# Kernel optimization log

Hardware: AMD Instinct MI355X
Metric: run time of the kernel (lower is better)

Reference implementation:

```python
import jax, jax.numpy as jnp
import numpy as np

D = 2048          # in_features == out_features (d_model)
H_TOTAL = 8192    # hidden_features, split across experts
E = 8             # num_experts
K = 2             # num_selects (top-k)
HE = H_TOTAL // E # per-expert hidden size
B, S = 2, 2048


def setup_inputs() -> dict:
    key = jax.random.key(0)
    ks = jax.random.split(key, 8)
    scale_up = 1.0 / np.sqrt(D)
    scale_dn = 1.0 / np.sqrt(HE)
    return {
        "x": jax.random.normal(ks[0], (B, S, D), dtype=jnp.float32),
        # mlp gate network: Linear(D,E,no bias) -> tanh -> Linear(E,E,no bias)
        "Wg1": jax.random.normal(ks[1], (E, D), dtype=jnp.float32) * 0.02,
        "Wg2": jax.random.normal(ks[2], (E, E), dtype=jnp.float32) * 0.2,
        # per-expert GLU-MLP weights (stacked over expert axis)
        "Wup": jax.random.uniform(ks[3], (E, HE, D), dtype=jnp.float32, minval=-scale_up, maxval=scale_up),
        "bup": jax.random.uniform(ks[4], (E, HE), dtype=jnp.float32, minval=-scale_up, maxval=scale_up),
        "Wdown": jax.random.uniform(ks[5], (E, D, HE), dtype=jnp.float32, minval=-scale_dn, maxval=scale_dn),
        "bdown": jax.random.uniform(ks[6], (E, D), dtype=jnp.float32, minval=-scale_dn, maxval=scale_dn),
    }


def reference(x, Wg1, Wg2, Wup, bup, Wdown, bdown):
    Bd, Sd, Dd = x.shape
    T = Bd * Sd
    xt = x.reshape(T, Dd)                                   # [T, D] tokens

    # ---- TopKBalancedNoisyGate (eval mode: no noise) ----
    logits = jnp.tanh(xt @ Wg1.T) @ Wg2.T                   # [T, E]
    _, top_idx = jax.lax.top_k(logits, K)                   # [T, K]
    top_logits = jnp.take_along_axis(logits, top_idx, axis=1)
    top_scores = jax.nn.softmax(top_logits.astype(jnp.float32), axis=1).astype(logits.dtype)
    # scatter top-k scores into dense [T, E] (zeros elsewhere)
    rows = jnp.arange(T)[:, None]
    scores = jnp.zeros_like(logits).at[rows, top_idx].set(top_scores)

    # ---- per-expert Linear-GLU experts: up -> silu -> down, score-combined ----
    up = jnp.einsum('td,ehd->teh', xt, Wup) + bup           # [T, E, HE]
    h = jax.nn.silu(up)
    down = jnp.einsum('teh,eoh->teo', h, Wdown) + bdown     # [T, E, D]
    out = jnp.einsum('te,teo->to', scores, down)            # [T, D]
    return out.reshape(Bd, Sd, Dd)
```

## Files before the change

### kernel.cpp

```cpp
#include <hip/hip_runtime.h>
#include <hip/hip_bf16.h>

#define D_DIM 2048
#define HE_DIM 1024
#define E_NUM 8
#define T_NUM 4096
#define TK_NUM 8192
#define TILE 128
#define BK 64
#define MAXROWS 9216
#define MAXMT 72

#define M_CNT(e)  ((e) * 32)
#define M_FILL(e) (256 + (e) * 32)
#define M_OFF  512
#define M_NMT  520
#define M_TE   528
#define M_TB   600
#define M_INTS 1024

typedef unsigned short u16;
typedef __attribute__((ext_vector_type(8))) short bf16x8;
typedef __attribute__((ext_vector_type(4))) float f32x4;

#define OFF_XB   ((size_t)0)
#define OFF_WUPB (OFF_XB + (size_t)T_NUM * D_DIM * 2)
#define OFF_SLOT ((size_t)0)
#define OFF_WDNB (OFF_WUPB + (size_t)E_NUM * HE_DIM * D_DIM * 2)
#define OFF_H    (OFF_WDNB + (size_t)E_NUM * D_DIM * HE_DIM * 2)
#define OFF_SCR  (OFF_H + (size_t)MAXROWS * HE_DIM * 2)
#define OFF_EIDX (OFF_SCR + (size_t)TK_NUM * 4)
#define OFF_RT   (OFF_EIDX + (size_t)TK_NUM * 4)
#define OFF_RS   (OFF_RT + (size_t)MAXROWS * 4)
#define OFF_META (OFF_RS + (size_t)MAXROWS * 4)

__device__ __forceinline__ u16 f2bf(float f) {
  unsigned u = __float_as_uint(f);
  u += 0x7FFFu + ((u >> 16) & 1u);
  return (u16)(u >> 16);
}
__device__ __forceinline__ float bf_lo(unsigned u) { return __uint_as_float(u << 16); }
__device__ __forceinline__ float bf_hi(unsigned u) { return __uint_as_float(u & 0xFFFF0000u); }

__device__ __forceinline__ void gload16(const void* g, void* l) {
  __builtin_amdgcn_global_load_lds((const __attribute__((address_space(1))) void*)g,
                                   (__attribute__((address_space(3))) void*)l,
                                   16, 0, 0);
}

__global__ void k_init(int* __restrict__ meta, int* __restrict__ rows_slot,
                       float* __restrict__ rowscore) {
  int i = blockIdx.x * blockDim.x + threadIdx.x;
  if (i < M_INTS) meta[i] = 0;
  if (i < MAXROWS) { rows_slot[i] = -1; rowscore[i] = 0.0f; }
}

__global__ void k_cvt2(const float4* __restrict__ s1, const float4* __restrict__ s2,
                       ushort4* __restrict__ d1, ushort4* __restrict__ d2, int n4) {
  int i = blockIdx.x * blockDim.x + threadIdx.x;
  int st = gridDim.x * blockDim.x;
  for (; i < 2 * n4; i += st) {
    const float4* s = (i < n4) ? s1 : s2;
    ushort4* d = (i < n4) ? d1 : d2;
    int j = (i < n4) ? i : i - n4;
    float4 v = s[j];
    ushort4 o;
    o.x = f2bf(v.x); o.y = f2bf(v.y); o.z = f2bf(v.z); o.w = f2bf(v.w);
    d[j] = o;
  }
}

__global__ __launch_bounds__(256) void k_gate(
    const float4* __restrict__ x4, const float4* __restrict__ Wg1_4,
    const float* __restrict__ Wg2, ushort4* __restrict__ xb4,
    int* __restrict__ eidx, float* __restrict__ scr, int* __restrict__ meta) {
  __shared__ float4 wg1s[E_NUM * (D_DIM / 4)];
  __shared__ int cnt_s[E_NUM];
  const int tid = threadIdx.x;
  if (tid < E_NUM) cnt_s[tid] = 0;
#pragma unroll
  for (int i = 0; i < 16; ++i) wg1s[tid + i * 256] = Wg1_4[tid + i * 256];
  __syncthreads();

  const int w = tid >> 6;
  const int lane = tid & 63;
  for (int j = 0; j < 4; ++j) {
    const int t = blockIdx.x * 16 + w * 4 + j;
    float acc[E_NUM];
#pragma unroll
    for (int e = 0; e < E_NUM; ++e) acc[e] = 0.f;
#pragma unroll
    for (int i = 0; i < 8; ++i) {
      const int c = lane + i * 64;
      float4 xv = x4[(size_t)t * 512 + c];
      ushort4 o;
      o.x = f2bf(xv.x); o.y = f2bf(xv.y); o.z = f2bf(xv.z); o.w = f2bf(xv.w);
      xb4[(size_t)t * 512 + c] = o;
#pragma unroll
      for (int e = 0; e < E_NUM; ++e) {
        float4 wv = wg1s[e * 512 + c];
        acc[e] += xv.x * wv.x + xv.y * wv.y + xv.z * wv.z + xv.w * wv.w;
      }
    }
#pragma unroll
    for (int e = 0; e < E_NUM; ++e) {
      float v = acc[e];
#pragma unroll
      for (int off = 32; off; off >>= 1) v += __shfl_xor(v, off, 64);
      acc[e] = v;
    }
    if (lane == 0) {
      float l1[E_NUM], lg[E_NUM];
#pragma unroll
      for (int e = 0; e < E_NUM; ++e) l1[e] = tanhf(acc[e]);
#pragma unroll
      for (int i = 0; i < E_NUM; ++i) {
        float s = 0.f;
#pragma unroll
        for (int e = 0; e < E_NUM; ++e) s += l1[e] * Wg2[i * E_NUM + e];
        lg[i] = s;
      }
      int i0 = 0; float v0 = lg[0];
#pragma unroll
      for (int i = 1; i < E_NUM; ++i) if (lg[i] > v0) { v0 = lg[i]; i0 = i; }
      int i1 = -1; float v1 = -3.4e38f;
#pragma unroll
      for (int i = 0; i < E_NUM; ++i) if (i != i0 && lg[i] > v1) { v1 = lg[i]; i1 = i; }
      float e1 = __expf(v1 - v0);
      float s0 = 1.f / (1.f + e1);
      float s1 = e1 * s0;
      eidx[t * 2] = i0; eidx[t * 2 + 1] = i1;
      scr[t * 2] = s0;  scr[t * 2 + 1] = s1;
      atomicAdd(&cnt_s[i0], 1);
      atomicAdd(&cnt_s[i1], 1);
    }
  }
  __syncthreads();
  if (tid < E_NUM) atomicAdd(&meta[M_CNT(tid)], cnt_s[tid]);
}

__global__ void k_offsets(int* __restrict__ meta) {
  const int lane = threadIdx.x;
  int cnt = (lane < E_NUM) ? meta[M_CNT(lane)] : 0;
  int tiles = (cnt + TILE - 1) / TILE;
  int pre = tiles;
#pragma unroll
  for (int off = 1; off < E_NUM; off <<= 1) {
    int v = __shfl_up(pre, off, 64);
    if (lane >= off && lane < E_NUM) pre += v;
  }
  int tb_excl = pre - tiles;
  if (lane < E_NUM) meta[M_OFF + lane] = tb_excl * TILE;
  const int nmt = __shfl(pre, E_NUM - 1, 64);
  if (lane == 0) meta[M_NMT] = nmt;
  int tb[E_NUM];
#pragma unroll
  for (int k = 0; k < E_NUM; ++k) tb[k] = __shfl(tb_excl, k, 64);
  for (int mt = lane; mt < nmt; mt += 64) {
    int e = 0;
#pragma unroll
    for (int k = 1; k < E_NUM; ++k) if (mt >= tb[k]) e = k;
    meta[M_TE + mt] = e;
    meta[M_TB + mt] = mt * TILE;
  }
}

__global__ void k_assign(const int* __restrict__ eidx, const float* __restrict__ scr,
                         int* __restrict__ meta, int* __restrict__ rows_slot,
                         float* __restrict__ rowscore) {
  int i = blockIdx.x * blockDim.x + threadIdx.x;
  const int lane = threadIdx.x & 63;
  int e = eidx[i];
  int pos = 0;
#pragma unroll
  for (int ex = 0; ex < E_NUM; ++ex) {
    unsigned long long m = __ballot(e == ex);
    if (e == ex) {
      int leader = __ffsll((long long)m) - 1;
      int rank = __popcll(m & ((1ull << lane) - 1ull));
      int b = 0;
      if (lane == leader) b = atomicAdd(&meta[M_FILL(ex)], __popcll(m));
      b = __shfl(b, leader, 64);
      pos = b + rank;
    }
  }
  int r = meta[M_OFF + e] + pos;
  rows_slot[r] = i;
  rowscore[r] = scr[i];
}

__global__ __launch_bounds__(256) void k_up(
    const u16* __restrict__ xb, const u16* __restrict__ wupb,
    const float* __restrict__ bup, const int* __restrict__ meta,
    const int* __restrict__ rows_slot, u16* __restrict__ hbuf) {
  const int mt = blockIdx.y;
  if (mt >= meta[M_NMT]) return;
  const int e = meta[M_TE + mt];
  const int mbase = meta[M_TB + mt];
  const int nt = blockIdx.x;

  __shared__ u16 As[TILE * BK];
  __shared__ u16 Bs[TILE * BK];

  const int tid = threadIdx.x;
  const int lane = tid & 63;
  const int w = tid >> 6;
  const int r0 = tid >> 3;
  const int cb = (((tid & 7) ^ ((tid >> 3) & 7)) * 8);

  const u16* gA[4];
  const u16* gB[4];
#pragma unroll
  for (int j = 0; j < 4; ++j) {
    int s = rows_slot[mbase + r0 + 32 * j]; if (s < 0) s = 0;
    gA[j] = xb + (size_t)(s >> 1) * D_DIM + cb;
    gB[j] = wupb + ((size_t)e * HE_DIM + nt * TILE + r0 + 32 * j) * D_DIM + cb;
  }
  u16* lA = As + tid * 8;
  u16* lB = Bs + tid * 8;

  const int wm = (w & 1) * 64;
  const int wn = (w >> 1) * 64;
  const int quad = lane >> 4;
  const int l16 = lane & 15;
  const int sw = l16 & 7;
  const u16* pa0 = As + (wm + l16) * BK;
  const u16* pb0 = Bs + (wn + l16) * BK;

  f32x4 acc[4][4] = {};

  for (int k0 = 0; k0 < D_DIM; k0 += BK) {
#pragma unroll
    for (int j = 0; j < 4; ++j) gload16(gA[j] + k0, lA + 2048 * j);
#pragma unroll
    for (int j = 0; j < 4; ++j) gload16(gB[j] + k0, lB + 2048 * j);
    __syncthreads();
#pragma unroll
    for (int h = 0; h < 2; ++h) {
      const int off = ((h * 4 + quad) ^ sw) * 8;
      bf16x8 af[4], bfr[4];
#pragma unroll
      for (int i = 0; i < 4; ++i) {
        af[i]  = *(const bf16x8*)(pa0 + i * 16 * BK + off);
        bfr[i] = *(const bf16x8*)(pb0 + i * 16 * BK + off);
      }
#pragma unroll
      for (int mi = 0; mi < 4; ++mi)
#pragma unroll
        for (int ni = 0; ni < 4; ++ni)
          acc[mi][ni] = __builtin_amdgcn_mfma_f32_16x16x32_bf16(af[mi], bfr[ni], acc[mi][ni], 0, 0, 0);
    }
    __syncthreads();
  }

#pragma unroll
  for (int mi = 0; mi < 4; ++mi) {
    const int m = wm + mi * 16 + quad * 4;
#pragma unroll
    for (int ni = 0; ni < 4; ++ni) {
      const int ng = nt * TILE + wn + ni * 16 + l16;
      const float bias = bup[e * HE_DIM + ng];
#pragma unroll
      for (int r = 0; r < 4; ++r) {
        float v = acc[mi][ni][r] + bias;
        v = v / (1.0f + __expf(-v));
        hbuf[(size_t)(mbase + m + r) * HE_DIM + ng] = f2bf(v);
      }
    }
  }
}

__global__ __launch_bounds__(256) void k_down(
    const u16* __restrict__ hbuf, const u16* __restrict__ wdnb,
    const float* __restrict__ bdown, const int* __restrict__ meta,
    const int* __restrict__ rows_slot, const float* __restrict__ rowscore,
    u16* __restrict__ slot) {
  const int mt = blockIdx.y;
  if (mt >= meta[M_NMT]) return;
  const int e = meta[M_TE + mt];
  const int mbase = meta[M_TB + mt];
  const int nt = blockIdx.x;

  __shared__ u16 As[TILE * BK];
  __shared__ u16 Bs[TILE * BK];

  const int tid = threadIdx.x;
  const int lane = tid & 63;
  const int w = tid >> 6;
  const int r0 = tid >> 3;
  const int cb = (((tid & 7) ^ ((tid >> 3) & 7)) * 8);

  const u16* gA[4];
  const u16* gB[4];
#pragma unroll
  for (int j = 0; j < 4; ++j) {
    gA[j] = hbuf + (size_t)(mbase + r0 + 32 * j) * HE_DIM + cb;
    gB[j] = wdnb + ((size_t)e * D_DIM + nt * TILE + r0 + 32 * j) * HE_DIM + cb;
  }
  u16* lA = As + tid * 8;
  u16* lB = Bs + tid * 8;

  const int wm = (w & 1) * 64;
  const int wn = (w >> 1) * 64;
  const int quad = lane >> 4;
  const int l16 = lane & 15;
  const int sw = l16 & 7;
  const u16* pa0 = As + (wm + l16) * BK;
  const u16* pb0 = Bs + (wn + l16) * BK;

  f32x4 acc[4][4] = {};

  for (int k0 = 0; k0 < HE_DIM; k0 += BK) {
#pragma unroll
    for (int j = 0; j < 4; ++j) gload16(gA[j] + k0, lA + 2048 * j);
#pragma unroll
    for (int j = 0; j < 4; ++j) gload16(gB[j] + k0, lB + 2048 * j);
    __syncthreads();
#pragma unroll
    for (int h = 0; h < 2; ++h) {
      const int off = ((h * 4 + quad) ^ sw) * 8;
      bf16x8 af[4], bfr[4];
#pragma unroll
      for (int i = 0; i < 4; ++i) {
        af[i]  = *(const bf16x8*)(pa0 + i * 16 * BK + off);
        bfr[i] = *(const bf16x8*)(pb0 + i * 16 * BK + off);
      }
#pragma unroll
      for (int mi = 0; mi < 4; ++mi)
#pragma unroll
        for (int ni = 0; ni < 4; ++ni)
          acc[mi][ni] = __builtin_amdgcn_mfma_f32_16x16x32_bf16(af[mi], bfr[ni], acc[mi][ni], 0, 0, 0);
    }
    __syncthreads();
  }

#pragma unroll
  for (int mi = 0; mi < 4; ++mi) {
    const int m = wm + mi * 16 + quad * 4;
#pragma unroll
    for (int r = 0; r < 4; ++r) {
      const int rg = mbase + m + r;
      const int s = rows_slot[rg];
      const float sc = rowscore[rg];
      if (s < 0) continue;
      u16* dst = slot + (size_t)s * D_DIM;
#pragma unroll
      for (int ni = 0; ni < 4; ++ni) {
        const int ng = nt * TILE + wn + ni * 16 + l16;
        float v = (acc[mi][ni][r] + bdown[e * D_DIM + ng]) * sc;
        dst[ng] = f2bf(v);
      }
    }
  }
}

__global__ __launch_bounds__(256) void k_combine(const u16* __restrict__ slot,
                                                 float* __restrict__ out) {
  int i = blockIdx.x * blockDim.x + threadIdx.x;
  int t = i >> 8;
  int c = i & 255;
  const uint4* p0 = (const uint4*)(slot + (size_t)(t * 2) * D_DIM) + c;
  const uint4* p1 = (const uint4*)(slot + (size_t)(t * 2 + 1) * D_DIM) + c;
  uint4 a = *p0, b = *p1;
  float4 o0, o1;
  o0.x = bf_lo(a.x) + bf_lo(b.x);  o0.y = bf_hi(a.x) + bf_hi(b.x);
  o0.z = bf_lo(a.y) + bf_lo(b.y);  o0.w = bf_hi(a.y) + bf_hi(b.y);
  o1.x = bf_lo(a.z) + bf_lo(b.z);  o1.y = bf_hi(a.z) + bf_hi(b.z);
  o1.z = bf_lo(a.w) + bf_lo(b.w);  o1.w = bf_hi(a.w) + bf_hi(b.w);
  float4* po = (float4*)(out + (size_t)t * D_DIM) + c * 2;
  po[0] = o0;
  po[1] = o1;
}

extern "C" void kernel_launch(void* const* d_in, const int* in_sizes, int n_in,
                              void* d_out, int out_size, void* d_ws, size_t ws_size,
                              hipStream_t stream) {
  const float* x     = (const float*)d_in[0];
  const float* Wg1   = (const float*)d_in[1];
  const float* Wg2   = (const float*)d_in[2];
  const float* Wup   = (const float*)d_in[3];
  const float* bup   = (const float*)d_in[4];
  const float* Wdown = (const float*)d_in[5];
  const float* bdown = (const float*)d_in[6];
  float* out = (float*)d_out;

  char* ws = (char*)d_ws;
  u16*   xb         = (u16*)(ws + OFF_XB);
  u16*   wupb       = (u16*)(ws + OFF_WUPB);
  u16*   wdnb       = (u16*)(ws + OFF_WDNB);
  u16*   hbuf       = (u16*)(ws + OFF_H);
  u16*   slotbuf    = (u16*)(ws + OFF_SLOT);
  float* scr        = (float*)(ws + OFF_SCR);
  int*   eidx       = (int*)(ws + OFF_EIDX);
  int*   rows_slot  = (int*)(ws + OFF_RT);
  float* rowscore   = (float*)(ws + OFF_RS);
  int*   meta       = (int*)(ws + OFF_META);

  k_init<<<(MAXROWS + 255) / 256, 256, 0, stream>>>(meta, rows_slot, rowscore);
  k_cvt2<<<8192, 256, 0, stream>>>((const float4*)Wup, (const float4*)Wdown,
                                   (ushort4*)wupb, (ushort4*)wdnb,
                                   E_NUM * HE_DIM * D_DIM / 4);
  k_gate<<<T_NUM / 16, 256, 0, stream>>>((const float4*)x, (const float4*)Wg1, Wg2,
                                         (ushort4*)xb, eidx, scr, meta);
  k_offsets<<<1, 64, 0, stream>>>(meta);
  k_assign<<<TK_NUM / 256, 256, 0, stream>>>(eidx, scr, meta, rows_slot, rowscore);
  k_up<<<dim3(HE_DIM / TILE, MAXMT), 256, 0, stream>>>(xb, wupb, bup, meta, rows_slot, hbuf);
  k_down<<<dim3(D_DIM / TILE, MAXMT), 256, 0, stream>>>(hbuf, wdnb, bdown, meta,
                                                        rows_slot, rowscore, slotbuf);
  k_combine<<<T_NUM * D_DIM / 8 / 256, 256, 0, stream>>>(slotbuf, out);
}
```

Measured before the change: 380.1 us.

## Double-buffer expert GEMMs with 512 threads and fold init/offset kernels into neighbors

The up and down expert GEMMs now use 512-thread blocks, where each wave covers a 64x32 sub-tile, and double-buffered LDS. The next K-slice is prefetched with global_load_lds while MFMAs run on the current slice, which removes one barrier per iteration. Separately, k_init is merged into the weight-conversion kernel, and k_offsets moves into the last block of k_gate through an atomic ticket, removing two launches. Risks: a larger LDS footprint, fewer MFMAs per wave relative to fragment loads, and a prefetch write into the other buffer without a wait on async loads before the barrier.

```diff
diff --git a/kernel.cpp b/kernel.cpp
--- a/kernel.cpp
+++ b/kernel.cpp
@@ -17,6 +17,7 @@
 #define M_NMT  520
 #define M_TE   528
 #define M_TB   600
+#define M_TICKET 704
 #define M_INTS 1024
 
 typedef unsigned short u16;
@@ -48,18 +49,15 @@
                                    16, 0, 0);
 }
 
-__global__ void k_init(int* __restrict__ meta, int* __restrict__ rows_slot,
+__global__ void k_cvt2(const float4* __restrict__ s1, const float4* __restrict__ s2,
+                       ushort4* __restrict__ d1, ushort4* __restrict__ d2, int n4,
+                       int* __restrict__ meta, int* __restrict__ rows_slot,
                        float* __restrict__ rowscore) {
-  int i = blockIdx.x * blockDim.x + threadIdx.x;
-  if (i < M_INTS) meta[i] = 0;
-  if (i < MAXROWS) { rows_slot[i] = -1; rowscore[i] = 0.0f; }
-}
-
-__global__ void k_cvt2(const float4* __restrict__ s1, const float4* __restrict__ s2,
-                       ushort4* __restrict__ d1, ushort4* __restrict__ d2, int n4) {
-  int i = blockIdx.x * blockDim.x + threadIdx.x;
-  int st = gridDim.x * blockDim.x;
-  for (; i < 2 * n4; i += st) {
+  const int i0 = blockIdx.x * blockDim.x + threadIdx.x;
+  if (i0 < M_INTS) meta[i0] = 0;
+  if (i0 < MAXROWS) { rows_slot[i0] = -1; rowscore[i0] = 0.0f; }
+  const int st = gridDim.x * blockDim.x;
+  for (int i = i0; i < 2 * n4; i += st) {
     const float4* s = (i < n4) ? s1 : s2;
     ushort4* d = (i < n4) ? d1 : d2;
     int j = (i < n4) ? i : i - n4;
@@ -76,6 +74,7 @@
     int* __restrict__ eidx, float* __restrict__ scr, int* __restrict__ meta) {
   __shared__ float4 wg1s[E_NUM * (D_DIM / 4)];
   __shared__ int cnt_s[E_NUM];
+  __shared__ int lastf;
   const int tid = threadIdx.x;
   if (tid < E_NUM) cnt_s[tid] = 0;
 #pragma unroll
@@ -137,31 +136,36 @@
   }
   __syncthreads();
   if (tid < E_NUM) atomicAdd(&meta[M_CNT(tid)], cnt_s[tid]);
-}
-
-__global__ void k_offsets(int* __restrict__ meta) {
-  const int lane = threadIdx.x;
-  int cnt = (lane < E_NUM) ? meta[M_CNT(lane)] : 0;
-  int tiles = (cnt + TILE - 1) / TILE;
-  int pre = tiles;
-#pragma unroll
-  for (int off = 1; off < E_NUM; off <<= 1) {
-    int v = __shfl_up(pre, off, 64);
-    if (lane >= off && lane < E_NUM) pre += v;
-  }
-  int tb_excl = pre - tiles;
-  if (lane < E_NUM) meta[M_OFF + lane] = tb_excl * TILE;
-  const int nmt = __shfl(pre, E_NUM - 1, 64);
-  if (lane == 0) meta[M_NMT] = nmt;
-  int tb[E_NUM];
-#pragma unroll
-  for (int k = 0; k < E_NUM; ++k) tb[k] = __shfl(tb_excl, k, 64);
-  for (int mt = lane; mt < nmt; mt += 64) {
-    int e = 0;
-#pragma unroll
-    for (int k = 1; k < E_NUM; ++k) if (mt >= tb[k]) e = k;
-    meta[M_TE + mt] = e;
-    meta[M_TB + mt] = mt * TILE;
+
+  if (tid == 0) {
+    __threadfence();
+    lastf = (atomicAdd(&meta[M_TICKET], 1) == (int)gridDim.x - 1);
+  }
+  __syncthreads();
+  if (lastf && tid < 64) {
+    const int l2 = tid;
+    int cnt = (l2 < E_NUM) ? atomicAdd(&meta[M_CNT(l2)], 0) : 0;
+    int tiles = (cnt + TILE - 1) / TILE;
+    int pre = tiles;
+#pragma unroll
+    for (int off = 1; off < E_NUM; off <<= 1) {
+      int v = __shfl_up(pre, off, 64);
+      if (l2 >= off && l2 < E_NUM) pre += v;
+    }
+    int tb_excl = pre - tiles;
+    if (l2 < E_NUM) meta[M_OFF + l2] = tb_excl * TILE;
+    const int nmt = __shfl(pre, E_NUM - 1, 64);
+    if (l2 == 0) meta[M_NMT] = nmt;
+    int tb[E_NUM];
+#pragma unroll
+    for (int k = 0; k < E_NUM; ++k) tb[k] = __shfl(tb_excl, k, 64);
+    for (int mt = l2; mt < nmt; mt += 64) {
+      int e = 0;
+#pragma unroll
+      for (int k = 1; k < E_NUM; ++k) if (mt >= tb[k]) e = k;
+      meta[M_TE + mt] = e;
+      meta[M_TB + mt] = mt * TILE;
+    }
   }
 }
 
@@ -189,7 +193,7 @@
   rowscore[r] = scr[i];
 }
 
-__global__ __launch_bounds__(256) void k_up(
+__global__ __launch_bounds__(512) void k_up(
     const u16* __restrict__ xb, const u16* __restrict__ wupb,
     const float* __restrict__ bup, const int* __restrict__ meta,
     const int* __restrict__ rows_slot, u16* __restrict__ hbuf) {
@@ -199,65 +203,68 @@
   const int mbase = meta[M_TB + mt];
   const int nt = blockIdx.x;
 
-  __shared__ u16 As[TILE * BK];
-  __shared__ u16 Bs[TILE * BK];
+  __shared__ u16 As[2][TILE * BK];
+  __shared__ u16 Bs[2][TILE * BK];
 
   const int tid = threadIdx.x;
   const int lane = tid & 63;
   const int w = tid >> 6;
   const int r0 = tid >> 3;
-  const int cb = (((tid & 7) ^ ((tid >> 3) & 7)) * 8);
-
-  const u16* gA[4];
-  const u16* gB[4];
-#pragma unroll
-  for (int j = 0; j < 4; ++j) {
-    int s = rows_slot[mbase + r0 + 32 * j]; if (s < 0) s = 0;
+  const int cb = (((tid & 7) ^ (r0 & 7)) * 8);
+
+  const u16* gA[2];
+  const u16* gB[2];
+#pragma unroll
+  for (int j = 0; j < 2; ++j) {
+    int s = rows_slot[mbase + r0 + 64 * j]; if (s < 0) s = 0;
     gA[j] = xb + (size_t)(s >> 1) * D_DIM + cb;
-    gB[j] = wupb + ((size_t)e * HE_DIM + nt * TILE + r0 + 32 * j) * D_DIM + cb;
-  }
-  u16* lA = As + tid * 8;
-  u16* lB = Bs + tid * 8;
+    gB[j] = wupb + ((size_t)e * HE_DIM + nt * TILE + r0 + 64 * j) * D_DIM + cb;
+  }
 
   const int wm = (w & 1) * 64;
-  const int wn = (w >> 1) * 64;
+  const int wn = (w >> 1) * 32;
   const int quad = lane >> 4;
   const int l16 = lane & 15;
   const int sw = l16 & 7;
-  const u16* pa0 = As + (wm + l16) * BK;
-  const u16* pb0 = Bs + (wn + l16) * BK;
-
-  f32x4 acc[4][4] = {};
-
+
+  f32x4 acc[4][2] = {};
+
+#define STAGE_UP(buf, k0) \
+  { gload16(gA[0] + (k0), &As[buf][tid * 8]);        \
+    gload16(gA[1] + (k0), &As[buf][tid * 8 + 4096]); \
+    gload16(gB[0] + (k0), &Bs[buf][tid * 8]);        \
+    gload16(gB[1] + (k0), &Bs[buf][tid * 8 + 4096]); }
+
+  STAGE_UP(0, 0);
+  __syncthreads();
+  int cur = 0;
   for (int k0 = 0; k0 < D_DIM; k0 += BK) {
-#pragma unroll
-    for (int j = 0; j < 4; ++j) gload16(gA[j] + k0, lA + 2048 * j);
-#pragma unroll
-    for (int j = 0; j < 4; ++j) gload16(gB[j] + k0, lB + 2048 * j);
-    __syncthreads();
+    if (k0 + BK < D_DIM) STAGE_UP(cur ^ 1, k0 + BK);
+    const u16* pa0 = &As[cur][(wm + l16) * BK];
+    const u16* pb0 = &Bs[cur][(wn + l16) * BK];
 #pragma unroll
     for (int h = 0; h < 2; ++h) {
       const int off = ((h * 4 + quad) ^ sw) * 8;
-      bf16x8 af[4], bfr[4];
-#pragma unroll
-      for (int i = 0; i < 4; ++i) {
-        af[i]  = *(const bf16x8*)(pa0 + i * 16 * BK + off);
-        bfr[i] = *(const bf16x8*)(pb0 + i * 16 * BK + off);
-      }
+      bf16x8 af[4], bfr[2];
+#pragma unroll
+      for (int i = 0; i < 4; ++i) af[i] = *(const bf16x8*)(pa0 + i * 16 * BK + off);
+#pragma unroll
+      for (int i = 0; i < 2; ++i) bfr[i] = *(const bf16x8*)(pb0 + i * 16 * BK + off);
 #pragma unroll
       for (int mi = 0; mi < 4; ++mi)
 #pragma unroll
-        for (int ni = 0; ni < 4; ++ni)
+        for (int ni = 0; ni < 2; ++ni)
           acc[mi][ni] = __builtin_amdgcn_mfma_f32_16x16x32_bf16(af[mi], bfr[ni], acc[mi][ni], 0, 0, 0);
     }
     __syncthreads();
+    cur ^= 1;
   }
 
 #pragma unroll
   for (int mi = 0; mi < 4; ++mi) {
     const int m = wm + mi * 16 + quad * 4;
 #pragma unroll
-    for (int ni = 0; ni < 4; ++ni) {
+    for (int ni = 0; ni < 2; ++ni) {
       const int ng = nt * TILE + wn + ni * 16 + l16;
       const float bias = bup[e * HE_DIM + ng];
 #pragma unroll
@@ -270,7 +277,7 @@
   }
 }
 
-__global__ __launch_bounds__(256) void k_down(
+__global__ __launch_bounds__(512) void k_down(
     const u16* __restrict__ hbuf, const u16* __restrict__ wdnb,
     const float* __restrict__ bdown, const int* __restrict__ meta,
     const int* __restrict__ rows_slot, const float* __restrict__ rowscore,
@@ -281,57 +288,60 @@
   const int mbase = meta[M_TB + mt];
   const int nt = blockIdx.x;
 
-  __shared__ u16 As[TILE * BK];
-  __shared__ u16 Bs[TILE * BK];
+  __shared__ u16 As[2][TILE * BK];
+  __shared__ u16 Bs[2][TILE * BK];
 
   const int tid = threadIdx.x;
   const int lane = tid & 63;
   const int w = tid >> 6;
   const int r0 = tid >> 3;
-  const int cb = (((tid & 7) ^ ((tid >> 3) & 7)) * 8);
-
-  const u16* gA[4];
-  const u16* gB[4];
-#pragma unroll
-  for (int j = 0; j < 4; ++j) {
-    gA[j] = hbuf + (size_t)(mbase + r0 + 32 * j) * HE_DIM + cb;
-    gB[j] = wdnb + ((size_t)e * D_DIM + nt * TILE + r0 + 32 * j) * HE_DIM + cb;
-  }
-  u16* lA = As + tid * 8;
-  u16* lB = Bs + tid * 8;
+  const int cb = (((tid & 7) ^ (r0 & 7)) * 8);
+
+  const u16* gA[2];
+  const u16* gB[2];
+#pragma unroll
+  for (int j = 0; j < 2; ++j) {
+    gA[j] = hbuf + (size_t)(mbase + r0 + 64 * j) * HE_DIM + cb;
+    gB[j] = wdnb + ((size_t)e * D_DIM + nt * TILE + r0 + 64 * j) * HE_DIM + cb;
+  }
 
   const int wm = (w & 1) * 64;
-  const int wn = (w >> 1) * 64;
+  const int wn = (w >> 1) * 32;
   const int quad = lane >> 4;
   const int l16 = lane & 15;
   const int sw = l16 & 7;
-  const u16* pa0 = As + (wm + l16) * BK;
-  const u16* pb0 = Bs + (wn + l16) * BK;
-
-  f32x4 acc[4][4] = {};
-
+
+  f32x4 acc[4][2] = {};
+
+#define STAGE_DN(buf, k0) \
+  { gload16(gA[0] + (k0), &As[buf][tid * 8]);        \
+    gload16(gA[1] + (k0), &As[buf][tid * 8 + 4096]); \
+    gload16(gB[0] + (k0), &Bs[buf][tid * 8]);        \
+    gload16(gB[1] + (k0), &Bs[buf][tid * 8 + 4096]); }
+
+  STAGE_DN(0, 0);
+  __syncthreads();
+  int cur = 0;
   for (int k0 = 0; k0 < HE_DIM; k0 += BK) {
-#pragma unroll
-    for (int j = 0; j < 4; ++j) gload16(gA[j] + k0, lA + 2048 * j);
-#pragma unroll
-    for (int j = 0; j < 4; ++j) gload16(gB[j] + k0, lB + 2048 * j);
-    __syncthreads();
+    if (k0 + BK < HE_DIM) STAGE_DN(cur ^ 1, k0 + BK);
+    const u16* pa0 = &As[cur][(wm + l16) * BK];
+    const u16* pb0 = &Bs[cur][(wn + l16) * BK];
 #pragma unroll
     for (int h = 0; h < 2; ++h) {
       const int off = ((h * 4 + quad) ^ sw) * 8;
-      bf16x8 af[4], bfr[4];
-#pragma unroll
-      for (int i = 0; i < 4; ++i) {
-        af[i]  = *(const bf16x8*)(pa0 + i * 16 * BK + off);
-        bfr[i] = *(const bf16x8*)(pb0 + i * 16 * BK + off);
-      }
+      bf16x8 af[4], bfr[2];
+#pragma unroll
+      for (int i = 0; i < 4; ++i) af[i] = *(const bf16x8*)(pa0 + i * 16 * BK + off);
+#pragma unroll
+      for (int i = 0; i < 2; ++i) bfr[i] = *(const bf16x8*)(pb0 + i * 16 * BK + off);
 #pragma unroll
       for (int mi = 0; mi < 4; ++mi)
 #pragma unroll
-        for (int ni = 0; ni < 4; ++ni)
+        for (int ni = 0; ni < 2; ++ni)
           acc[mi][ni] = __builtin_amdgcn_mfma_f32_16x16x32_bf16(af[mi], bfr[ni], acc[mi][ni], 0, 0, 0);
     }
     __syncthreads();
+    cur ^= 1;
   }
 
 #pragma unroll
@@ -345,7 +355,7 @@
       if (s < 0) continue;
       u16* dst = slot + (size_t)s * D_DIM;
 #pragma unroll
-      for (int ni = 0; ni < 4; ++ni) {
+      for (int ni = 0; ni < 2; ++ni) {
         const int ng = nt * TILE + wn + ni * 16 + l16;
         float v = (acc[mi][ni][r] + bdown[e * D_DIM + ng]) * sc;
         dst[ng] = f2bf(v);
@@ -396,16 +406,15 @@
   float* rowscore   = (float*)(ws + OFF_RS);
   int*   meta       = (int*)(ws + OFF_META);
 
-  k_init<<<(MAXROWS + 255) / 256, 256, 0, stream>>>(meta, rows_slot, rowscore);
   k_cvt2<<<8192, 256, 0, stream>>>((const float4*)Wup, (const float4*)Wdown,
                                    (ushort4*)wupb, (ushort4*)wdnb,
-                                   E_NUM * HE_DIM * D_DIM / 4);
+                                   E_NUM * HE_DIM * D_DIM / 4,
+                                   meta, rows_slot, rowscore);
   k_gate<<<T_NUM / 16, 256, 0, stream>>>((const float4*)x, (const float4*)Wg1, Wg2,
                                          (ushort4*)xb, eidx, scr, meta);
-  k_offsets<<<1, 64, 0, stream>>>(meta);
   k_assign<<<TK_NUM / 256, 256, 0, stream>>>(eidx, scr, meta, rows_slot, rowscore);
-  k_up<<<dim3(HE_DIM / TILE, MAXMT), 256, 0, stream>>>(xb, wupb, bup, meta, rows_slot, hbuf);
-  k_down<<<dim3(D_DIM / TILE, MAXMT), 256, 0, stream>>>(hbuf, wdnb, bdown, meta,
+  k_up<<<dim3(HE_DIM / TILE, MAXMT), 512, 0, stream>>>(xb, wupb, bup, meta, rows_slot, hbuf);
+  k_down<<<dim3(D_DIM / TILE, MAXMT), 512, 0, stream>>>(hbuf, wdnb, bdown, meta,
                                                         rows_slot, rowscore, slotbuf);
   k_combine<<<T_NUM * D_DIM / 8 / 256, 256, 0, stream>>>(slotbuf, out);
 }
```

After: 365.7 us. -3.8%, faster.
